# Performance work log

Hardware: AMD Instinct MI355X
Metric: run time of the kernel (lower is better)

The kernel has to match this reference:

```python
import jax, jax.numpy as jnp
import numpy as np

B, T, E, H = 2, 2048, 1024, 16
D = E // H            # head dim = 64
ROT = D // 2          # rotary_dim = 32 (only first half of head dim is rotated)
THETA = 10000.0


def _rope(x):
    # x: (B, H, T, D). Faithful to rotary_embedding_torch.rotate_queries_or_keys
    # with dim=ROT: rotate first ROT features, interleaved-pair style, pass rest.
    t = x.shape[-2]
    inv = 1.0 / (THETA ** (jnp.arange(0, ROT, 2, dtype=jnp.float32) / ROT))   # (ROT//2,)
    freqs = jnp.arange(t, dtype=jnp.float32)[:, None] * inv[None, :]          # (T, ROT//2)
    freqs = jnp.repeat(freqs, 2, axis=-1)                                      # (T, ROT)
    cos, sin = jnp.cos(freqs), jnp.sin(freqs)
    xr, xp = x[..., :ROT], x[..., ROT:]
    p = xr.reshape(*xr.shape[:-1], ROT // 2, 2)
    rot = jnp.stack((-p[..., 1], p[..., 0]), axis=-1).reshape(xr.shape)
    return jnp.concatenate([xr * cos + rot * sin, xp], axis=-1)


def setup_inputs() -> dict:
    key = jax.random.key(0)
    k1, k2, k3 = jax.random.split(key, 3)
    query = jax.random.normal(k1, (B, T, E), dtype=jnp.float32)
    inputs = {
        "query": query,
        "key": query,            # ignored (cross_attention=False)
        "value": query,          # ignored
        "padding_mask": jnp.ones((B, T), dtype=bool),
        "in_proj_weight": jax.random.uniform(k2, (3 * E, E), dtype=jnp.float32),
        "out_proj_weight": jax.random.normal(k3, (E, E), dtype=jnp.float32) * (E ** -0.5),
    }
    return inputs


def reference(query, key, value, padding_mask, in_proj_weight, out_proj_weight):
    # cross_attention=False: key/value are overwritten by query
    key = query
    value = query
    q = query @ in_proj_weight[:E].T
    k = key @ in_proj_weight[E:2 * E].T
    v = value @ in_proj_weight[2 * E:].T
    # NOTE: raw reshape (B,T,E)->(B,H,T,D), exactly as in the torch module
    q = q.reshape(B, H, T, D)
    k = k.reshape(B, H, T, D)
    v = v.reshape(B, H, T, D)
    q = _rope(q)
    k = _rope(k)   # causal self-attention path: rotate keys too
    causal = jnp.tril(jnp.ones((T, T), dtype=bool))                 # (T, T)
    mask = causal[None, None] & padding_mask[:, None, None, :]      # (B,1,T,T) -> broadcast over H
    scores = jnp.einsum("bhqd,bhkd->bhqk", q, k) / jnp.sqrt(jnp.float32(D))
    scores = jnp.where(mask, scores, -jnp.inf)
    attn = jax.nn.softmax(scores, axis=-1)
    x = jnp.einsum("bhqk,bhkd->bhqd", attn, v)
    x = x.reshape(B, T, E)      # raw reshape back, as in torch
    return x @ out_proj_weight.T
```

## Files before the change

kernel.cpp:

```cpp
#include <hip/hip_runtime.h>
#include <stdint.h>

#define T_ 2048
#define E_ 1024

typedef __attribute__((ext_vector_type(8))) __bf16 bf16x8;
typedef __attribute__((ext_vector_type(4))) float f32x4;

__device__ __forceinline__ void gload_lds16(const void* g, void* l) {
  __builtin_amdgcn_global_load_lds(
      (const __attribute__((address_space(1))) unsigned int*)g,
      (__attribute__((address_space(3))) unsigned int*)l, 16, 0, 0);
}

__global__ __launch_bounds__(256) void k_prep(const float4* __restrict__ q,
                                              ushort4* __restrict__ xh,
                                              ushort4* __restrict__ xl,
                                              const float4* __restrict__ win,
                                              ushort4* __restrict__ whh,
                                              ushort4* __restrict__ whl,
                                              const float4* __restrict__ wout,
                                              ushort4* __restrict__ wob,
                                              float2* __restrict__ cs) {
  const int b = blockIdx.x, tid = threadIdx.x;
  if (b < 7168) {
    const float4* src;
    ushort4 *hi, *lo;
    int i;
    if (b < 4096) { src = q; hi = xh; lo = xl; i = b * 256 + tid; }
    else          { src = win; hi = whh; lo = whl; i = (b - 4096) * 256 + tid; }
    float4 x = src[i];
    float xs[4] = {x.x, x.y, x.z, x.w};
    union { __bf16 bb[4]; ushort4 u; } H, L;
#pragma unroll
    for (int jj = 0; jj < 4; ++jj) {
      __bf16 h = (__bf16)xs[jj];
      H.bb[jj] = h;
      L.bb[jj] = (__bf16)(xs[jj] - (float)h);
    }
    hi[i] = H.u;
    lo[i] = L.u;
  } else if (b < 8192) {
    int i = (b - 7168) * 256 + tid;
    float4 x = wout[i];
    float xs[4] = {x.x, x.y, x.z, x.w};
    union { __bf16 bb[4]; ushort4 u; } H;
#pragma unroll
    for (int jj = 0; jj < 4; ++jj) H.bb[jj] = (__bf16)xs[jj];
    wob[i] = H.u;
  } else {
    int i = (b - 8192) * 256 + tid;
    int t = i >> 4, f = i & 15;
    double inv = pow(10000.0, -(double)f / 16.0);
    double ang = (double)t * inv;
    cs[i] = make_float2((float)cos(ang), (float)sin(ang));
  }
}

template <int EPI, bool HILO>
__global__ __launch_bounds__(256) void k_gemm(const __bf16* __restrict__ Ah,
                                              const __bf16* __restrict__ Al,
                                              const __bf16* __restrict__ Bh,
                                              const __bf16* __restrict__ Bl,
                                              int M, int N, int K,
                                              const float2* __restrict__ cs,
                                              __bf16* __restrict__ qhi,
                                              __bf16* __restrict__ qlo,
                                              __bf16* __restrict__ khi,
                                              __bf16* __restrict__ klo,
                                              __bf16* __restrict__ v16,
                                              float* __restrict__ C32) {
  __shared__ __align__(16) __bf16 AsH[128 * 32];
  __shared__ __align__(16) __bf16 BsH[128 * 32];
  __shared__ __align__(16) __bf16 AsL[HILO ? 128 * 32 : 4];
  __shared__ __align__(16) __bf16 BsL[HILO ? 128 * 32 : 4];
  const int tid = threadIdx.x, lane = tid & 63, w = tid >> 6;
  const int wm = w >> 1, wn = w & 1;
  const int g = lane >> 4, d = lane & 15;
  const int m0 = blockIdx.y * 128, n0 = blockIdx.x * 128;

  f32x4 acc[4][4];
#pragma unroll
  for (int i = 0; i < 4; ++i)
#pragma unroll
    for (int j = 0; j < 4; ++j) acc[i][j] = (f32x4)(0.0f);

  const int row0 = tid >> 2, kc = tid & 3;
  const int row1 = 64 + row0;

  for (int k0 = 0; k0 < K; k0 += 32) {
    __syncthreads();
    gload_lds16(Ah + (size_t)(m0 + row0) * K + k0 + kc * 8, &AsH[w * 512]);
    gload_lds16(Ah + (size_t)(m0 + row1) * K + k0 + kc * 8, &AsH[2048 + w * 512]);
    gload_lds16(Bh + (size_t)(n0 + row0) * K + k0 + kc * 8, &BsH[w * 512]);
    gload_lds16(Bh + (size_t)(n0 + row1) * K + k0 + kc * 8, &BsH[2048 + w * 512]);
    if constexpr (HILO) {
      gload_lds16(Al + (size_t)(m0 + row0) * K + k0 + kc * 8, &AsL[w * 512]);
      gload_lds16(Al + (size_t)(m0 + row1) * K + k0 + kc * 8, &AsL[2048 + w * 512]);
      gload_lds16(Bl + (size_t)(n0 + row0) * K + k0 + kc * 8, &BsL[w * 512]);
      gload_lds16(Bl + (size_t)(n0 + row1) * K + k0 + kc * 8, &BsL[2048 + w * 512]);
    }
    __syncthreads();
    bf16x8 ah[4], bh[4], al[4], bl[4];
#pragma unroll
    for (int i = 0; i < 4; ++i) {
      ah[i] = *(const bf16x8*)&AsH[(wm * 64 + i * 16 + d) * 32 + g * 8];
      bh[i] = *(const bf16x8*)&BsH[(wn * 64 + i * 16 + d) * 32 + g * 8];
      if constexpr (HILO) {
        al[i] = *(const bf16x8*)&AsL[(wm * 64 + i * 16 + d) * 32 + g * 8];
        bl[i] = *(const bf16x8*)&BsL[(wn * 64 + i * 16 + d) * 32 + g * 8];
      }
    }
#pragma unroll
    for (int i = 0; i < 4; ++i)
#pragma unroll
      for (int j = 0; j < 4; ++j) {
        acc[i][j] = __builtin_amdgcn_mfma_f32_16x16x32_bf16(ah[i], bh[j], acc[i][j], 0, 0, 0);
        if constexpr (HILO) {
          acc[i][j] = __builtin_amdgcn_mfma_f32_16x16x32_bf16(al[i], bh[j], acc[i][j], 0, 0, 0);
          acc[i][j] = __builtin_amdgcn_mfma_f32_16x16x32_bf16(ah[i], bl[j], acc[i][j], 0, 0, 0);
        }
      }
  }

#pragma unroll
  for (int i = 0; i < 4; ++i) {
    const int rbase = m0 + wm * 64 + i * 16 + g * 4;
#pragma unroll
    for (int j = 0; j < 4; ++j) {
      const int col = n0 + wn * 64 + j * 16 + d;
#pragma unroll
      for (int r = 0; r < 4; ++r) {
        const float vv = acc[i][j][r];
        const int row = rbase + r;
        if constexpr (EPI == 0) {
          const float xp = __shfl_xor(vv, 1);
          const int which = col >> 10;
          const int cl = col & 1023;
          const int d2 = cl & 63;
          const int t2 = (row & 127) * 16 + (cl >> 6);
          float y;
          if (d2 < 32) {
            const float2 cse = cs[t2 * 16 + (d2 >> 1)];
            y = (d2 & 1) ? (vv * cse.x + xp * cse.y) : (vv * cse.x - xp * cse.y);
          } else {
            y = vv;
          }
          if (which == 0) y *= 0.18033688011112042f;
          const __bf16 hi = (__bf16)y;
          const __bf16 lo = (__bf16)(y - (float)hi);
          const size_t off = (size_t)row * 1024 + cl;
          (which ? khi : qhi)[off] = hi;
          (which ? klo : qlo)[off] = lo;
        } else if constexpr (EPI == 1) {
          C32[(size_t)row * N + col] = vv;
        } else {
          v16[(size_t)row * N + col] = (__bf16)vv;
        }
      }
    }
  }
}

template <int EPI>
__global__ __launch_bounds__(256) void k_gemm64(const __bf16* __restrict__ Ah,
                                                const __bf16* __restrict__ Bh,
                                                int M, int N, int K,
                                                __bf16* __restrict__ v16,
                                                float* __restrict__ C32) {
  __shared__ __align__(16) __bf16 As[64 * 32];
  __shared__ __align__(16) __bf16 Bs[128 * 32];
  const int tid = threadIdx.x, lane = tid & 63, w = tid >> 6;
  const int g = lane >> 4, d = lane & 15;
  const int m0 = blockIdx.y * 64, n0 = blockIdx.x * 128;

  f32x4 acc[4][2];
#pragma unroll
  for (int i = 0; i < 4; ++i)
#pragma unroll
    for (int j = 0; j < 2; ++j) acc[i][j] = (f32x4)(0.0f);

  const int row0 = tid >> 2, kc = tid & 3;
  const int row1 = 64 + row0;

  for (int k0 = 0; k0 < K; k0 += 32) {
    __syncthreads();
    gload_lds16(Ah + (size_t)(m0 + row0) * K + k0 + kc * 8, &As[w * 512]);
    gload_lds16(Bh + (size_t)(n0 + row0) * K + k0 + kc * 8, &Bs[w * 512]);
    gload_lds16(Bh + (size_t)(n0 + row1) * K + k0 + kc * 8, &Bs[2048 + w * 512]);
    __syncthreads();
    bf16x8 ah[4], bh[2];
#pragma unroll
    for (int i = 0; i < 4; ++i) ah[i] = *(const bf16x8*)&As[(i * 16 + d) * 32 + g * 8];
#pragma unroll
    for (int j = 0; j < 2; ++j)
      bh[j] = *(const bf16x8*)&Bs[(w * 32 + j * 16 + d) * 32 + g * 8];
#pragma unroll
    for (int i = 0; i < 4; ++i)
#pragma unroll
      for (int j = 0; j < 2; ++j)
        acc[i][j] = __builtin_amdgcn_mfma_f32_16x16x32_bf16(ah[i], bh[j], acc[i][j], 0, 0, 0);
  }

#pragma unroll
  for (int i = 0; i < 4; ++i) {
    const int rbase = m0 + i * 16 + g * 4;
#pragma unroll
    for (int j = 0; j < 2; ++j) {
      const int col = n0 + w * 32 + j * 16 + d;
#pragma unroll
      for (int r = 0; r < 4; ++r) {
        const int row = rbase + r;
        if constexpr (EPI == 1) C32[(size_t)row * N + col] = acc[i][j][r];
        else v16[(size_t)row * N + col] = (__bf16)acc[i][j][r];
      }
    }
  }
}

__global__ __launch_bounds__(256) void k_vtrans(const __bf16* __restrict__ v16,
                                                __bf16* __restrict__ v16t) {
  __shared__ __bf16 TB[64][72];
  const int p = blockIdx.y, t0 = blockIdx.x * 64;
  const int tid = threadIdx.x;
  const int r = tid >> 2, c4 = (tid & 3) * 16;
  const __bf16* src = v16 + ((size_t)p * 2048 + t0 + r) * 64 + c4;
  bf16x8 A = *(const bf16x8*)src;
  bf16x8 B2 = *(const bf16x8*)(src + 8);
#pragma unroll
  for (int e = 0; e < 8; ++e) {
    TB[c4 + e][r] = A[e];
    TB[c4 + 8 + e][r] = B2[e];
  }
  __syncthreads();
  const int dd = tid >> 2, cc = (tid & 3) * 16;
  __bf16* dst = v16t + ((size_t)p * 64 + dd) * 2048 + t0 + cc;
  *(bf16x8*)dst = *(const bf16x8*)&TB[dd][cc];
  *(bf16x8*)(dst + 8) = *(const bf16x8*)&TB[dd][cc + 8];
}

__device__ __forceinline__ void find_unit(int W, int& qt, int& j) {
  qt = 0;
#pragma unroll
  for (int q = 1; q <= 7; ++q)
    if (40 * q * q + 16 * q <= W) qt = q;
  int s = 40 * qt * qt + 16 * qt;
  j = 0;
  while (s < W) {
    int p = j - 4 * qt;
    s += (p < 0) ? 20 : 20 - 4 * p;
    ++j;
  }
}

__global__ __launch_bounds__(512, 4) void k_attn(const __bf16* __restrict__ qhi,
                                                 const __bf16* __restrict__ qlo,
                                                 const __bf16* __restrict__ khi,
                                                 const __bf16* __restrict__ klo,
                                                 const __bf16* __restrict__ v16t,
                                                 __bf16* __restrict__ x16,
                                                 float* __restrict__ po,
                                                 float* __restrict__ pm,
                                                 float* __restrict__ pl_) {
  __shared__ __align__(16) __bf16 KH[2][64 * 64];
  __shared__ __align__(16) __bf16 KL[2][64 * 64];
  __shared__ __align__(16) __bf16 VT[2][64 * 64];
  __shared__ __align__(16) __bf16 PL[8][16 * 72];

  const int b = blockIdx.x, panel = blockIdx.y;
  int qtA, jA, qtE, jE;
  find_unit(168 * b, qtA, jA);
  find_unit(168 * (b + 1), qtE, jE);
  int nseg, jhi0, jhi1 = 0;
  if (qtE == qtA)      { nseg = 1; jhi0 = jE - 1; }
  else if (jE == 0)    { nseg = 1; jhi0 = 4 * qtA + 3; }
  else                 { nseg = 2; jhi0 = 4 * qtA + 3; jhi1 = jE - 1; }

  const int tid = threadIdx.x, lane = tid & 63, w = tid >> 6;
  const int g = lane >> 4, d = lane & 15;
  const size_t hb = (size_t)panel * T_ * 64;

  const int kr = tid >> 3, kc = tid & 7;
  const int swz = (kc ^ (kr & 7)) * 8;
  const __bf16* kB = khi + hb;
  const __bf16* lB = klo + hb;
  const __bf16* vB = v16t + (size_t)panel * (64 * T_);

#define STAGE(j, bb)                                                        \
  {                                                                         \
    gload_lds16(kB + (size_t)((j) * 64 + kr) * 64 + swz, &KH[bb][w * 512]); \
    gload_lds16(lB + (size_t)((j) * 64 + kr) * 64 + swz, &KL[bb][w * 512]); \
    gload_lds16(vB + (size_t)kr * T_ + (j) * 64 + swz, &VT[bb][w * 512]);   \
  }

  int cur = 0;
  STAGE(jA, 0);

#pragma unroll
  for (int seg = 0; seg < 2; ++seg) {
    if (seg >= nseg) break;
    const int qt = qtA + seg;
    const int jlo = seg ? 0 : jA;
    const int jhi = seg ? jhi1 : jhi0;
    const int q0 = qt << 8;

    bf16x8 qh[2][2], ql[2][2];
#pragma unroll
    for (int rb = 0; rb < 2; ++rb) {
      const int rbi = w * 2 + rb;
      const size_t qrow = hb + (size_t)(q0 + rbi * 16 + d) * 64;
      qh[rb][0] = *(const bf16x8*)&qhi[qrow + g * 8];
      qh[rb][1] = *(const bf16x8*)&qhi[qrow + 32 + g * 8];
      ql[rb][0] = *(const bf16x8*)&qlo[qrow + g * 8];
      ql[rb][1] = *(const bf16x8*)&qlo[qrow + 32 + g * 8];
    }

    f32x4 o[2][4];
#pragma unroll
    for (int rb = 0; rb < 2; ++rb)
#pragma unroll
      for (int i = 0; i < 4; ++i) o[rb][i] = (f32x4)(0.0f);
    float m_[2] = {-__builtin_inff(), -__builtin_inff()};
    float l_[2] = {0.0f, 0.0f};

    for (int j = jlo; j <= jhi; ++j) {
      __syncthreads();
      if (j < jhi) {
        STAGE(j + 1, cur ^ 1);
      } else if (!seg && nseg == 2) {
        STAGE(0, cur ^ 1);
      }

#pragma unroll
      for (int rb = 0; rb < 2; ++rb) {
        const int rbi = w * 2 + rb;
        const int qrow0 = q0 + rbi * 16;
        if (j * 64 > qrow0 + 15) continue;

        f32x4 s[4];
        __builtin_amdgcn_s_setprio(1);
#pragma unroll
        for (int f = 0; f < 4; ++f) {
          f32x4 accs = (f32x4)(0.0f);
          const int colr = f * 16 + d;
#pragma unroll
          for (int ds = 0; ds < 2; ++ds) {
            const int slot = ((ds * 4 + g) ^ (colr & 7)) * 8;
            const bf16x8 kf = *(const bf16x8*)&KH[cur][colr * 64 + slot];
            const bf16x8 lf = *(const bf16x8*)&KL[cur][colr * 64 + slot];
            accs = __builtin_amdgcn_mfma_f32_16x16x32_bf16(kf, qh[rb][ds], accs, 0, 0, 0);
            accs = __builtin_amdgcn_mfma_f32_16x16x32_bf16(kf, ql[rb][ds], accs, 0, 0, 0);
            accs = __builtin_amdgcn_mfma_f32_16x16x32_bf16(lf, qh[rb][ds], accs, 0, 0, 0);
          }
          s[f] = accs;
        }
        __builtin_amdgcn_s_setprio(0);

        if (j * 64 + 63 > qrow0) {
          const int qq = qrow0 + d;
#pragma unroll
          for (int f = 0; f < 4; ++f)
#pragma unroll
            for (int r = 0; r < 4; ++r) {
              const int kv = j * 64 + f * 16 + g * 4 + r;
              if (kv > qq) s[f][r] = -30000.0f;
            }
        }

        float pmax = fmaxf(fmaxf(s[0][0], s[0][1]), fmaxf(s[0][2], s[0][3]));
#pragma unroll
        for (int f = 1; f < 4; ++f)
          pmax = fmaxf(pmax, fmaxf(fmaxf(s[f][0], s[f][1]), fmaxf(s[f][2], s[f][3])));
        pmax = fmaxf(pmax, __shfl_xor(pmax, 16));
        pmax = fmaxf(pmax, __shfl_xor(pmax, 32));

        if (!__all(pmax - m_[rb] <= 11.5f)) {
          const float mnew = fmaxf(m_[rb], pmax);
          const float fac = exp2f(m_[rb] - mnew);
          m_[rb] = mnew;
          float facr[4];
#pragma unroll
          for (int r = 0; r < 4; ++r)
            facr[r] = __shfl(fac, (lane & 48) | (g * 4 + r));
#pragma unroll
          for (int ni = 0; ni < 4; ++ni)
#pragma unroll
            for (int r = 0; r < 4; ++r) o[rb][ni][r] *= facr[r];
          l_[rb] *= fac;
        }

        float sum = 0.0f;
#pragma unroll
        for (int f = 0; f < 4; ++f) {
          union { __bf16 bb[4]; ushort4 u4; } pk;
#pragma unroll
          for (int r = 0; r < 4; ++r) {
            const float pv = exp2f(s[f][r] - m_[rb]);
            sum += pv;
            pk.bb[r] = (__bf16)pv;
          }
          *(ushort4*)&PL[w][d * 72 + f * 16 + g * 4] = pk.u4;
        }
        sum += __shfl_xor(sum, 16);
        sum += __shfl_xor(sum, 32);
        l_[rb] += sum;

        __builtin_amdgcn_s_setprio(1);
#pragma unroll
        for (int ks = 0; ks < 2; ++ks) {
          const bf16x8 pa = *(const bf16x8*)&PL[w][d * 72 + ks * 32 + g * 8];
#pragma unroll
          for (int ni = 0; ni < 4; ++ni) {
            const bf16x8 vf =
                *(const bf16x8*)&VT[cur][(ni * 16 + d) * 64 + (((ks * 4 + g) ^ (d & 7)) * 8)];
            o[rb][ni] = __builtin_amdgcn_mfma_f32_16x16x32_bf16(pa, vf, o[rb][ni], 0, 0, 0);
          }
        }
        __builtin_amdgcn_s_setprio(0);
      }
      cur ^= 1;
    }

    const int slot = panel * 23 + b + qt;
#pragma unroll
    for (int rb = 0; rb < 2; ++rb) {
      const int rbi = w * 2 + rb;
#pragma unroll
      for (int ni = 0; ni < 4; ++ni)
#pragma unroll
        for (int r = 0; r < 4; ++r) {
          const int rowin = rbi * 16 + g * 4 + r;
          po[(size_t)slot * 16384 + rowin * 64 + ni * 16 + d] = o[rb][ni][r];
        }
      if (g == 0) {
        pm[slot * 256 + rbi * 16 + d] = m_[rb];
        pl_[slot * 256 + rbi * 16 + d] = l_[rb];
      }
    }
  }
#undef STAGE
}

__global__ __launch_bounds__(256) void k_combine(const float* __restrict__ po,
                                                 const float* __restrict__ pm,
                                                 const float* __restrict__ pl_,
                                                 __bf16* __restrict__ x16) {
  const int p = blockIdx.y;
  const int li = blockIdx.x * 256 + threadIdx.x;
  const int d = li & 63;
  const int t2 = li >> 6;
  const int qt = t2 >> 8;
  const int rowin = t2 & 255;
  const int cq = 40 * qt * qt + 16 * qt;
  const int nc = (cq + 80 * qt + 48) / 168 - cq / 168 + 1;
  const int s0 = p * 23 + cq / 168 + qt;
  float M = -__builtin_inff();
  for (int s = 0; s < nc; ++s) M = fmaxf(M, pm[(s0 + s) * 256 + rowin]);
  float L = 0.0f, O = 0.0f;
  for (int s = 0; s < nc; ++s) {
    const float ww = exp2f(pm[(s0 + s) * 256 + rowin] - M);
    L += pl_[(s0 + s) * 256 + rowin] * ww;
    O += po[(size_t)(s0 + s) * 16384 + rowin * 64 + d] * ww;
  }
  x16[((size_t)p * T_ + t2) * 64 + d] = (__bf16)(O / L);
}

extern "C" void kernel_launch(void* const* d_in, const int* in_sizes, int n_in,
                              void* d_out, int out_size, void* d_ws, size_t ws_size,
                              hipStream_t stream) {
  const float* query = (const float*)d_in[0];
  const float* win = (const float*)d_in[4];
  const float* wout = (const float*)d_in[5];
  float* out = (float*)d_out;

  const size_t MB = 1024 * 1024;
  const size_t KB = 1024;
  char* ws = (char*)d_ws;
  __bf16* xh = (__bf16*)(ws);
  __bf16* xl = (__bf16*)(ws + 8 * MB);
  __bf16* whh = (__bf16*)(ws + 16 * MB);
  __bf16* whl = (__bf16*)(ws + 22 * MB);
  __bf16* wob = (__bf16*)(ws + 28 * MB);
  float* pm = (float*)(ws + 30 * MB);
  float* pl_ = (float*)(ws + 30 * MB + 768 * KB);
  float2* cs = (float2*)(ws + 31 * MB + 512 * KB);
  float* po = (float*)(ws + 32 * MB);
  __bf16* qhi = (__bf16*)(ws + 78 * MB);
  __bf16* qlo = (__bf16*)(ws + 86 * MB);
  __bf16* khi = (__bf16*)(ws + 94 * MB);
  __bf16* klo = (__bf16*)(ws + 102 * MB);
  __bf16* x16 = (__bf16*)(ws + 78 * MB);
  __bf16* v16 = (__bf16*)(ws + 64 * MB);
  __bf16* v16t = (__bf16*)(ws);

  k_prep<<<8320, 256, 0, stream>>>((const float4*)query, (ushort4*)xh, (ushort4*)xl,
                                   (const float4*)win, (ushort4*)whh, (ushort4*)whl,
                                   (const float4*)wout, (ushort4*)wob, cs);

  dim3 gqk(16, 32);
  k_gemm<0, true><<<gqk, 256, 0, stream>>>(xh, xl, whh, whl, 4096, 2048, 1024, cs,
                                           qhi, qlo, khi, klo, nullptr, nullptr);
  dim3 gv(8, 64);
  k_gemm64<2><<<gv, 256, 0, stream>>>(xh, whh + (size_t)2048 * 1024, 4096, 1024, 1024,
                                      v16, nullptr);

  dim3 gt(32, 32);
  k_vtrans<<<gt, 256, 0, stream>>>(v16, v16t);

  dim3 ga(16, 32);
  k_attn<<<ga, 512, 0, stream>>>(qhi, qlo, khi, klo, v16t, x16, po, pm, pl_);

  dim3 gc(512, 32);
  k_combine<<<gc, 256, 0, stream>>>(po, pm, pl_, x16);

  dim3 go(8, 64);
  k_gemm64<1><<<go, 256, 0, stream>>>(x16, wob, 4096, 1024, 1024, nullptr, out);
}
```

Measured before the change: 211.7 us.

## Rebalance attention work by KV-tile count and write complete q-tiles directly

Replaces the weighted work-split (find_unit with per-tile costs) with a simpler split that gives each block exactly 9 KV tiles across the causal q-tile sequence. When a block covers an entire q-tile, it normalizes and writes bf16 output directly instead of emitting partials. The combine kernel then skips the first q-tile, which is always complete. This cuts partial-buffer traffic and combine work, but ignores the lower cost of diagonal tiles, which may slightly unbalance the blocks.

```diff
diff --git a/kernel.cpp b/kernel.cpp
--- a/kernel.cpp
+++ b/kernel.cpp
@@ -239,20 +239,6 @@
   *(bf16x8*)(dst + 8) = *(const bf16x8*)&TB[dd][cc + 8];
 }
 
-__device__ __forceinline__ void find_unit(int W, int& qt, int& j) {
-  qt = 0;
-#pragma unroll
-  for (int q = 1; q <= 7; ++q)
-    if (40 * q * q + 16 * q <= W) qt = q;
-  int s = 40 * qt * qt + 16 * qt;
-  j = 0;
-  while (s < W) {
-    int p = j - 4 * qt;
-    s += (p < 0) ? 20 : 20 - 4 * p;
-    ++j;
-  }
-}
-
 __global__ __launch_bounds__(512, 4) void k_attn(const __bf16* __restrict__ qhi,
                                                  const __bf16* __restrict__ qlo,
                                                  const __bf16* __restrict__ khi,
@@ -268,13 +254,15 @@
   __shared__ __align__(16) __bf16 PL[8][16 * 72];
 
   const int b = blockIdx.x, panel = blockIdx.y;
-  int qtA, jA, qtE, jE;
-  find_unit(168 * b, qtA, jA);
-  find_unit(168 * (b + 1), qtE, jE);
-  int nseg, jhi0, jhi1 = 0;
-  if (qtE == qtA)      { nseg = 1; jhi0 = jE - 1; }
-  else if (jE == 0)    { nseg = 1; jhi0 = 4 * qtA + 3; }
-  else                 { nseg = 2; jhi0 = 4 * qtA + 3; jhi1 = jE - 1; }
+  const int u0 = 9 * b;
+  int qtA = 0;
+  while (2 * (qtA + 1) * (qtA + 2) <= u0) ++qtA;
+  const int cumA = 2 * qtA * (qtA + 1);
+  const int cumB = 2 * (qtA + 1) * (qtA + 2);
+  const int jloA = u0 - cumA;
+  const bool two = (u0 + 9 > cumB);
+  const int jhiA = two ? (cumB - 1 - cumA) : (u0 + 8 - cumA);
+  const int jhiB = u0 + 8 - cumB;
 
   const int tid = threadIdx.x, lane = tid & 63, w = tid >> 6;
   const int g = lane >> 4, d = lane & 15;
@@ -294,14 +282,13 @@
   }
 
   int cur = 0;
-  STAGE(jA, 0);
-
-#pragma unroll
+  STAGE(jloA, 0);
+
   for (int seg = 0; seg < 2; ++seg) {
-    if (seg >= nseg) break;
+    if (seg && !two) break;
     const int qt = qtA + seg;
-    const int jlo = seg ? 0 : jA;
-    const int jhi = seg ? jhi1 : jhi0;
+    const int jlo = seg ? 0 : jloA;
+    const int jhi = seg ? jhiB : jhiA;
     const int q0 = qt << 8;
 
     bf16x8 qh[2][2], ql[2][2];
@@ -327,7 +314,7 @@
       __syncthreads();
       if (j < jhi) {
         STAGE(j + 1, cur ^ 1);
-      } else if (!seg && nseg == 2) {
+      } else if (!seg && two) {
         STAGE(0, cur ^ 1);
       }
 
@@ -421,20 +408,38 @@
       cur ^= 1;
     }
 
-    const int slot = panel * 23 + b + qt;
-#pragma unroll
-    for (int rb = 0; rb < 2; ++rb) {
-      const int rbi = w * 2 + rb;
-#pragma unroll
-      for (int ni = 0; ni < 4; ++ni)
-#pragma unroll
-        for (int r = 0; r < 4; ++r) {
-          const int rowin = rbi * 16 + g * 4 + r;
-          po[(size_t)slot * 16384 + rowin * 64 + ni * 16 + d] = o[rb][ni][r];
-        }
-      if (g == 0) {
-        pm[slot * 256 + rbi * 16 + d] = m_[rb];
-        pl_[slot * 256 + rbi * 16 + d] = l_[rb];
+    if (jlo == 0 && jhi == 4 * qt + 3) {
+#pragma unroll
+      for (int rb = 0; rb < 2; ++rb) {
+        const int rbi = w * 2 + rb;
+        float lr[4];
+#pragma unroll
+        for (int r = 0; r < 4; ++r)
+          lr[r] = __shfl(l_[rb], (lane & 48) | (g * 4 + r));
+#pragma unroll
+        for (int ni = 0; ni < 4; ++ni)
+#pragma unroll
+          for (int r = 0; r < 4; ++r) {
+            const size_t row = hb + (size_t)(q0 + rbi * 16 + g * 4 + r) * 64;
+            x16[row + ni * 16 + d] = (__bf16)(o[rb][ni][r] / lr[r]);
+          }
+      }
+    } else {
+      const int slot = panel * 23 + b + qt;
+#pragma unroll
+      for (int rb = 0; rb < 2; ++rb) {
+        const int rbi = w * 2 + rb;
+#pragma unroll
+        for (int ni = 0; ni < 4; ++ni)
+#pragma unroll
+          for (int r = 0; r < 4; ++r) {
+            const int rowin = rbi * 16 + g * 4 + r;
+            po[(size_t)slot * 16384 + rowin * 64 + ni * 16 + d] = o[rb][ni][r];
+          }
+        if (g == 0) {
+          pm[slot * 256 + rbi * 16 + d] = m_[rb];
+          pl_[slot * 256 + rbi * 16 + d] = l_[rb];
+        }
       }
     }
   }
@@ -448,12 +453,12 @@
   const int p = blockIdx.y;
   const int li = blockIdx.x * 256 + threadIdx.x;
   const int d = li & 63;
-  const int t2 = li >> 6;
+  const int t2 = 256 + (li >> 6);
   const int qt = t2 >> 8;
   const int rowin = t2 & 255;
-  const int cq = 40 * qt * qt + 16 * qt;
-  const int nc = (cq + 80 * qt + 48) / 168 - cq / 168 + 1;
-  const int s0 = p * 23 + cq / 168 + qt;
+  const int cq = 2 * qt * (qt + 1);
+  const int nc = (cq + 4 * qt + 3) / 9 - cq / 9 + 1;
+  const int s0 = p * 23 + cq / 9 + qt;
   float M = -__builtin_inff();
   for (int s = 0; s < nc; ++s) M = fmaxf(M, pm[(s0 + s) * 256 + rowin]);
   float L = 0.0f, O = 0.0f;
@@ -510,7 +515,7 @@
   dim3 ga(16, 32);
   k_attn<<<ga, 512, 0, stream>>>(qhi, qlo, khi, klo, v16t, x16, po, pm, pl_);
 
-  dim3 gc(512, 32);
+  dim3 gc(448, 32);
   k_combine<<<gc, 256, 0, stream>>>(po, pm, pl_, x16);
 
   dim3 go(8, 64);
```

New measurement: 204.7 us. -3.3%, faster.
